# Optimization experiments

Hardware: AMD Instinct MI355X
Metric: run time of the kernel (lower is better)

## Reference

```python
import jax, jax.numpy as jnp
import numpy as np

DECAY = 0.99
EPS = 1e-05
DIM = 64
N_EMBED = 512
X_SHAPE = (32, 4096, DIM)


def setup_inputs() -> dict:
    key = jax.random.key(0)
    k1, k2 = jax.random.split(key)
    x = jax.random.normal(k1, X_SHAPE, dtype=jnp.float32)
    # codebook init uniform(-1/n_embed, 1/n_embed), as in torch .uniform_
    embed = jax.random.uniform(k2, (DIM, N_EMBED), dtype=jnp.float32,
                               minval=-1.0 / N_EMBED, maxval=1.0 / N_EMBED)
    cluster_size = jnp.zeros((N_EMBED,), dtype=jnp.float32)
    embed_avg = embed.copy()
    return {"x": x, "embed": embed, "cluster_size": cluster_size, "embed_avg": embed_avg}


def reference(x, embed, cluster_size, embed_avg):
    dim, n_embed = embed.shape
    flatten = x.reshape(-1, dim)  # [N, dim]
    # squared euclidean distance to each code: ||f||^2 - 2 f.E + ||E||^2  -> [N, n_embed]
    dist = (jnp.sum(flatten * flatten, axis=1, keepdims=True)
            - 2.0 * (flatten @ embed)
            + jnp.sum(embed * embed, axis=0, keepdims=True))
    embed_ind_flat = jnp.argmin(dist, axis=1)  # [N]
    embed_ind = embed_ind_flat.reshape(x.shape[:-1])
    quantize = jnp.take(embed.T, embed_ind_flat, axis=0).reshape(x.shape)

    # --- training-mode EMA buffer updates (no gradient flows; torch uses .data) ---
    f_sg = jax.lax.stop_gradient(flatten)
    # onehot.sum(0) == histogram of assignments; flatten.T @ onehot == segment_sum
    onehot_sum = jnp.zeros((n_embed,), dtype=x.dtype).at[embed_ind_flat].add(1.0)
    embed_sum = jax.ops.segment_sum(f_sg, embed_ind_flat, num_segments=n_embed).T  # [dim, n_embed]
    new_cluster_size = cluster_size * DECAY + (1.0 - DECAY) * onehot_sum
    new_embed_avg = embed_avg * DECAY + (1.0 - DECAY) * embed_sum
    n = jnp.sum(new_cluster_size)
    cs = (new_cluster_size + EPS) / (n + n_embed * EPS) * n
    new_embed = new_embed_avg / cs[None, :]

    diff = jnp.mean(jnp.square(jax.lax.stop_gradient(quantize) - x))
    quantize_st = x + jax.lax.stop_gradient(quantize - x)  # straight-through
    return quantize_st, diff, embed_ind, new_embed, new_cluster_size, new_embed_avg
```

## Files before the change

### kernel.cpp

```cpp
#include <hip/hip_runtime.h>

#define NVEC  131072
#define DIM   64
#define K     512
#define DECAYF 0.99f
#define OMDF   0.01f
#define EPSF   1e-5f
#define VPB   128
#define NBLK_ASSIGN (NVEC / VPB)

#define Q_OFF    0
#define DIFF_OFF 8388608
#define IND_OFF  8388609
#define NE_OFF   8519681
#define NCS_OFF  8552449
#define NEA_OFF  8552961

#define ET_OFF    0
#define C_OFF     32768
#define DPART_OFF 33280
#define INDI_OFF  35328
#define PCNT_OFF  166400
#define PESUM_OFF 168448
#define NSH_OFF   299520

__global__ __launch_bounds__(256) void vq_prep(const float* __restrict__ embed,
                                               float* __restrict__ ws) {
    #pragma clang fp contract(off)
    int j = blockIdx.x * 256 + threadIdx.x;
    float c = 0.0f;
    for (int d = 0; d < DIM; ++d) {
        float v = embed[d * K + j];
        ws[ET_OFF + j * DIM + d] = v;
        float t = v * v;
        c = c + t;
    }
    ws[C_OFF + j] = c;
}

__global__ __launch_bounds__(256)
__attribute__((amdgpu_waves_per_eu(3)))
void vq_assign(
    const float* __restrict__ x,
    const float* __restrict__ ET,
    const float* __restrict__ C,
    int*   __restrict__ indI,
    float* __restrict__ dpart,
    float* __restrict__ out)
{
    #pragma clang fp contract(off)
    __shared__ float sda[4][64], sdb[4][64];
    __shared__ int   sia[4][64], sib[4][64];
    __shared__ int   sba[64], sbb[64];
    __shared__ float wdl[4];

    int lane = threadIdx.x & 63;
    int wq   = __builtin_amdgcn_readfirstlane(threadIdx.x >> 6);
    int va   = blockIdx.x * VPB + lane;
    int vb   = va + 64;
    const float* fxa = x + (size_t)va * DIM;
    const float* fxb = x + (size_t)vb * DIM;

    float fa[DIM], fb[DIM];
    #pragma unroll
    for (int k = 0; k < DIM / 4; ++k) {
        float4 t = ((const float4*)fxa)[k];
        fa[4*k+0] = t.x; fa[4*k+1] = t.y; fa[4*k+2] = t.z; fa[4*k+3] = t.w;
    }
    #pragma unroll
    for (int k = 0; k < DIM / 4; ++k) {
        float4 t = ((const float4*)fxb)[k];
        fb[4*k+0] = t.x; fb[4*k+1] = t.y; fb[4*k+2] = t.z; fb[4*k+3] = t.w;
    }

    #define PIN16(a, b) asm volatile("" \
        : "+v"(a[(b)+0]),  "+v"(a[(b)+1]),  "+v"(a[(b)+2]),  "+v"(a[(b)+3]), \
          "+v"(a[(b)+4]),  "+v"(a[(b)+5]),  "+v"(a[(b)+6]),  "+v"(a[(b)+7]), \
          "+v"(a[(b)+8]),  "+v"(a[(b)+9]),  "+v"(a[(b)+10]), "+v"(a[(b)+11]), \
          "+v"(a[(b)+12]), "+v"(a[(b)+13]), "+v"(a[(b)+14]), "+v"(a[(b)+15]))
    PIN16(fa, 0); PIN16(fa, 16); PIN16(fa, 32); PIN16(fa, 48);
    PIN16(fb, 0); PIN16(fb, 16); PIN16(fb, 32); PIN16(fb, 48);
    #undef PIN16

    float ra[8], rb[8];
    #pragma unroll
    for (int k = 0; k < 8; ++k) { ra[k] = fa[k] * fa[k]; rb[k] = fb[k] * fb[k]; }
    #pragma unroll
    for (int b = 1; b < 8; ++b) {
        #pragma unroll
        for (int k = 0; k < 8; ++k) {
            float t0 = fa[8*b + k] * fa[8*b + k];
            ra[k] = ra[k] + t0;
            float t1 = fb[8*b + k] * fb[8*b + k];
            rb[k] = rb[k] + t1;
        }
    }
    float Aa = ((ra[0] + ra[1]) + (ra[2] + ra[3])) + ((ra[4] + ra[5]) + (ra[6] + ra[7]));
    float Ab = ((rb[0] + rb[1]) + (rb[2] + rb[3])) + ((rb[4] + rb[5]) + (rb[6] + rb[7]));

    const float* eseg = ET + (size_t)wq * 128 * DIM;
    const float* Cseg = C + wq * 128;
    float bda = 3.0e38f, bdb = 3.0e38f;
    int   bia = wq * 128, bib = wq * 128;
    #pragma unroll 1
    for (int jj = 0; jj < 128; ++jj) {
        const float* e = eseg + jj * DIM;
        float ma = 0.0f, mb = 0.0f;
        #pragma unroll
        for (int d = 0; d < DIM; ++d) {
            float ev = e[d];
            ma = __builtin_fmaf(fa[d], ev, ma);
            mb = __builtin_fmaf(fb[d], ev, mb);
        }
        int j = wq * 128 + jj;
        float Cv = Cseg[jj];
        float t1a = 2.0f * ma;
        float t2a = Aa - t1a;
        float da  = t2a + Cv;
        float t1b = 2.0f * mb;
        float t2b = Ab - t1b;
        float db  = t2b + Cv;
        if (da < bda) { bda = da; bia = j; }
        if (db < bdb) { bdb = db; bib = j; }
    }

    sda[wq][lane] = bda; sia[wq][lane] = bia;
    sdb[wq][lane] = bdb; sib[wq][lane] = bib;
    __syncthreads();

    if (wq == 0) {
        float bd = sda[0][lane]; int bi = sia[0][lane];
        #pragma unroll
        for (int q = 1; q < 4; ++q) {
            float d2 = sda[q][lane]; int i2 = sia[q][lane];
            if (d2 < bd || (d2 == bd && i2 < bi)) { bd = d2; bi = i2; }
        }
        sba[lane] = bi;
        out[IND_OFF + va] = (float)bi;
        indI[va] = bi;

        bd = sdb[0][lane]; bi = sib[0][lane];
        #pragma unroll
        for (int q = 1; q < 4; ++q) {
            float d2 = sdb[q][lane]; int i2 = sib[q][lane];
            if (d2 < bd || (d2 == bd && i2 < bi)) { bd = d2; bi = i2; }
        }
        sbb[lane] = bi;
        out[IND_OFF + vb] = (float)bi;
        indI[vb] = bi;
    }
    __syncthreads();

    float dl = 0.0f;
    if (wq == 0) {
        int bsel = sba[lane];
        const float4* qr = (const float4*)(ET + (size_t)bsel * DIM);
        float4* orow = (float4*)(out + Q_OFF + (size_t)va * DIM);
        #pragma unroll
        for (int k = 0; k < 16; ++k) {
            float4 tq = qr[k];
            float r0 = tq.x - fa[4*k+0];
            float r1 = tq.y - fa[4*k+1];
            float r2 = tq.z - fa[4*k+2];
            float r3 = tq.w - fa[4*k+3];
            dl = __builtin_fmaf(r0, r0, dl); dl = __builtin_fmaf(r1, r1, dl);
            dl = __builtin_fmaf(r2, r2, dl); dl = __builtin_fmaf(r3, r3, dl);
            orow[k] = tq;
        }
    } else if (wq == 1) {
        int bsel = sbb[lane];
        const float4* qr = (const float4*)(ET + (size_t)bsel * DIM);
        float4* orow = (float4*)(out + Q_OFF + (size_t)vb * DIM);
        #pragma unroll
        for (int k = 0; k < 16; ++k) {
            float4 tq = qr[k];
            float r0 = tq.x - fb[4*k+0];
            float r1 = tq.y - fb[4*k+1];
            float r2 = tq.z - fb[4*k+2];
            float r3 = tq.w - fb[4*k+3];
            dl = __builtin_fmaf(r0, r0, dl); dl = __builtin_fmaf(r1, r1, dl);
            dl = __builtin_fmaf(r2, r2, dl); dl = __builtin_fmaf(r3, r3, dl);
            orow[k] = tq;
        }
    }

    #pragma unroll
    for (int off = 32; off > 0; off >>= 1) dl += __shfl_down(dl, off);
    if (lane == 0) wdl[wq] = dl;
    __syncthreads();
    if (threadIdx.x == 0)
        dpart[blockIdx.x] = ((wdl[0] + wdl[1]) + (wdl[2] + wdl[3]));
}

__global__ __launch_bounds__(512) void vq_stats(
    const float* __restrict__ x,
    const int* __restrict__ indI,
    float* __restrict__ pcnt,
    float* __restrict__ pesum)
{
    __shared__ float p[8][DIM];
    __shared__ float c[8];
    int j    = blockIdx.x >> 2;
    int q    = blockIdx.x & 3;
    int lane = threadIdx.x & 63;
    int w    = __builtin_amdgcn_readfirstlane(threadIdx.x >> 6);

    int seg  = q * 8 + w;
    int base = seg * (NVEC / 32);

    float acc = 0.0f;
    int   cnt = 0;
    for (int i = 0; i < NVEC / 32; i += 256) {
        int4 idv = ((const int4*)(indI + base + i))[lane];
        unsigned long long m0 = __ballot(idv.x == j);
        unsigned long long m1 = __ballot(idv.y == j);
        unsigned long long m2 = __ballot(idv.z == j);
        unsigned long long m3 = __ballot(idv.w == j);
        cnt += (int)(__popcll(m0) + __popcll(m1) + __popcll(m2) + __popcll(m3));
        while (m0) { int b = __builtin_ctzll(m0); m0 &= m0 - 1;
                     acc += x[(size_t)(base + i + 4*b + 0) * DIM + lane]; }
        while (m1) { int b = __builtin_ctzll(m1); m1 &= m1 - 1;
                     acc += x[(size_t)(base + i + 4*b + 1) * DIM + lane]; }
        while (m2) { int b = __builtin_ctzll(m2); m2 &= m2 - 1;
                     acc += x[(size_t)(base + i + 4*b + 2) * DIM + lane]; }
        while (m3) { int b = __builtin_ctzll(m3); m3 &= m3 - 1;
                     acc += x[(size_t)(base + i + 4*b + 3) * DIM + lane]; }
    }
    p[w][lane] = acc;
    if (lane == 0) c[w] = (float)cnt;
    __syncthreads();
    if (w == 0) {
        float s = ((p[0][lane] + p[1][lane]) + (p[2][lane] + p[3][lane]))
                + ((p[4][lane] + p[5][lane]) + (p[6][lane] + p[7][lane]));
        pesum[((size_t)q * K + j) * DIM + lane] = s;
        if (lane == 0)
            pcnt[q * K + j] = ((c[0] + c[1]) + (c[2] + c[3]))
                            + ((c[4] + c[5]) + (c[6] + c[7]));
    }
}

__global__ __launch_bounds__(512) void vq_finalize1(
    const float* __restrict__ cluster_size,
    float* __restrict__ ws,
    float* __restrict__ out)
{
    __shared__ float wsum[8];
    __shared__ float dsum_sh[8];
    int j = threadIdx.x;

    float cj = ((ws[PCNT_OFF + 0*K + j] + ws[PCNT_OFF + 1*K + j])
              + (ws[PCNT_OFF + 2*K + j] + ws[PCNT_OFF + 3*K + j]));
    float ncs = DECAYF * cluster_size[j] + OMDF * cj;
    out[NCS_OFF + j] = ncs;

    float dsum = 0.0f;
    #pragma unroll
    for (int k = 0; k < NBLK_ASSIGN / 512; ++k)
        dsum += ws[DPART_OFF + k * 512 + j];

    float s = ncs;
    #pragma unroll
    for (int off = 32; off > 0; off >>= 1) {
        s    += __shfl_down(s, off);
        dsum += __shfl_down(dsum, off);
    }
    if ((j & 63) == 0) { wsum[j >> 6] = s; dsum_sh[j >> 6] = dsum; }
    __syncthreads();
    if (j == 0) {
        float n = 0.f, dtot = 0.f;
        #pragma unroll
        for (int w = 0; w < 8; ++w) { n += wsum[w]; dtot += dsum_sh[w]; }
        ws[NSH_OFF] = n;
        out[DIFF_OFF] = dtot * (1.0f / 8388608.0f);
    }
}

__global__ __launch_bounds__(512) void vq_finalize2(
    const float* __restrict__ embed_avg,
    const float* __restrict__ ws,
    float* __restrict__ out)
{
    int d = blockIdx.x;
    int j = threadIdx.x;

    float ncs = out[NCS_OFF + j];
    float n   = ws[NSH_OFF];
    float csz = (ncs + EPSF) / (n + (float)K * EPSF) * n;

    float es = ((ws[PESUM_OFF + ((size_t)0*K + j) * DIM + d]
               + ws[PESUM_OFF + ((size_t)1*K + j) * DIM + d])
              + (ws[PESUM_OFF + ((size_t)2*K + j) * DIM + d]
               + ws[PESUM_OFF + ((size_t)3*K + j) * DIM + d]));
    float ea = DECAYF * embed_avg[d * K + j] + OMDF * es;
    out[NEA_OFF + d * K + j] = ea;
    out[NE_OFF  + d * K + j] = ea / csz;
}

extern "C" void kernel_launch(void* const* d_in, const int* in_sizes, int n_in,
                              void* d_out, int out_size, void* d_ws, size_t ws_size,
                              hipStream_t stream) {
    const float* x            = (const float*)d_in[0];
    const float* embed        = (const float*)d_in[1];
    const float* cluster_size = (const float*)d_in[2];
    const float* embed_avg    = (const float*)d_in[3];
    float* out = (float*)d_out;
    float* ws  = (float*)d_ws;
    int*   indI = (int*)(ws + INDI_OFF);

    vq_prep<<<K / 256, 256, 0, stream>>>(embed, ws);
    vq_assign<<<NBLK_ASSIGN, 256, 0, stream>>>(
        x, ws + ET_OFF, ws + C_OFF, indI, ws + DPART_OFF, out);
    vq_stats<<<K * 4, 512, 0, stream>>>(
        x, indI, ws + PCNT_OFF, ws + PESUM_OFF);
    vq_finalize1<<<1, K, 0, stream>>>(cluster_size, ws, out);
    vq_finalize2<<<DIM, K, 0, stream>>>(embed_avg, ws, out);
}
```

Baseline: 262.8 us.

## Process four codes per stats block and fuse the two finalize kernels

The stats kernel now handles four codebook entries per block. Each loaded index vector is tested against all four codes, which cuts the re-reads of the index array and the block count by four. The two finalize kernels become one: every block recomputes the new cluster sizes and their total, so one launch and one global round trip go away. In exchange each block does fewer, more serial ballot loops, and the total reduction is done redundantly in all 64 finalize blocks.

New measurement: 268.8 us. +2.3%, slower.

```diff
diff --git a/kernel.cpp b/kernel.cpp
--- a/kernel.cpp
+++ b/kernel.cpp
@@ -198,65 +198,85 @@
     float* __restrict__ pcnt,
     float* __restrict__ pesum)
 {
-    __shared__ float p[8][DIM];
-    __shared__ float c[8];
-    int j    = blockIdx.x >> 2;
+    __shared__ float p[4][8][DIM];
+    __shared__ float c[4][8];
+    int jg   = blockIdx.x >> 2;
     int q    = blockIdx.x & 3;
     int lane = threadIdx.x & 63;
     int w    = __builtin_amdgcn_readfirstlane(threadIdx.x >> 6);
+    int j0   = jg * 4;
 
     int seg  = q * 8 + w;
     int base = seg * (NVEC / 32);
 
-    float acc = 0.0f;
-    int   cnt = 0;
+    float acc[4] = {0.0f, 0.0f, 0.0f, 0.0f};
+    int   cnt[4] = {0, 0, 0, 0};
     for (int i = 0; i < NVEC / 32; i += 256) {
         int4 idv = ((const int4*)(indI + base + i))[lane];
-        unsigned long long m0 = __ballot(idv.x == j);
-        unsigned long long m1 = __ballot(idv.y == j);
-        unsigned long long m2 = __ballot(idv.z == j);
-        unsigned long long m3 = __ballot(idv.w == j);
-        cnt += (int)(__popcll(m0) + __popcll(m1) + __popcll(m2) + __popcll(m3));
-        while (m0) { int b = __builtin_ctzll(m0); m0 &= m0 - 1;
-                     acc += x[(size_t)(base + i + 4*b + 0) * DIM + lane]; }
-        while (m1) { int b = __builtin_ctzll(m1); m1 &= m1 - 1;
-                     acc += x[(size_t)(base + i + 4*b + 1) * DIM + lane]; }
-        while (m2) { int b = __builtin_ctzll(m2); m2 &= m2 - 1;
-                     acc += x[(size_t)(base + i + 4*b + 2) * DIM + lane]; }
-        while (m3) { int b = __builtin_ctzll(m3); m3 &= m3 - 1;
-                     acc += x[(size_t)(base + i + 4*b + 3) * DIM + lane]; }
-    }
-    p[w][lane] = acc;
-    if (lane == 0) c[w] = (float)cnt;
+        #pragma unroll
+        for (int jj = 0; jj < 4; ++jj) {
+            int j = j0 + jj;
+            unsigned long long m0 = __ballot(idv.x == j);
+            unsigned long long m1 = __ballot(idv.y == j);
+            unsigned long long m2 = __ballot(idv.z == j);
+            unsigned long long m3 = __ballot(idv.w == j);
+            cnt[jj] += (int)(__popcll(m0) + __popcll(m1)
+                           + __popcll(m2) + __popcll(m3));
+            while (m0) { int b = __builtin_ctzll(m0); m0 &= m0 - 1;
+                         acc[jj] += x[(size_t)(base + i + 4*b + 0) * DIM + lane]; }
+            while (m1) { int b = __builtin_ctzll(m1); m1 &= m1 - 1;
+                         acc[jj] += x[(size_t)(base + i + 4*b + 1) * DIM + lane]; }
+            while (m2) { int b = __builtin_ctzll(m2); m2 &= m2 - 1;
+                         acc[jj] += x[(size_t)(base + i + 4*b + 2) * DIM + lane]; }
+            while (m3) { int b = __builtin_ctzll(m3); m3 &= m3 - 1;
+                         acc[jj] += x[(size_t)(base + i + 4*b + 3) * DIM + lane]; }
+        }
+    }
+    #pragma unroll
+    for (int jj = 0; jj < 4; ++jj) {
+        p[jj][w][lane] = acc[jj];
+        if (lane == 0) c[jj][w] = (float)cnt[jj];
+    }
     __syncthreads();
     if (w == 0) {
-        float s = ((p[0][lane] + p[1][lane]) + (p[2][lane] + p[3][lane]))
-                + ((p[4][lane] + p[5][lane]) + (p[6][lane] + p[7][lane]));
-        pesum[((size_t)q * K + j) * DIM + lane] = s;
-        if (lane == 0)
-            pcnt[q * K + j] = ((c[0] + c[1]) + (c[2] + c[3]))
-                            + ((c[4] + c[5]) + (c[6] + c[7]));
-    }
-}
-
-__global__ __launch_bounds__(512) void vq_finalize1(
+        #pragma unroll
+        for (int jj = 0; jj < 4; ++jj) {
+            float s = ((p[jj][0][lane] + p[jj][1][lane])
+                     + (p[jj][2][lane] + p[jj][3][lane]))
+                    + ((p[jj][4][lane] + p[jj][5][lane])
+                     + (p[jj][6][lane] + p[jj][7][lane]));
+            pesum[((size_t)q * K + (j0 + jj)) * DIM + lane] = s;
+            if (lane == 0)
+                pcnt[q * K + (j0 + jj)] =
+                    ((c[jj][0] + c[jj][1]) + (c[jj][2] + c[jj][3]))
+                  + ((c[jj][4] + c[jj][5]) + (c[jj][6] + c[jj][7]));
+        }
+    }
+}
+
+__global__ __launch_bounds__(512) void vq_finalize(
     const float* __restrict__ cluster_size,
-    float* __restrict__ ws,
+    const float* __restrict__ embed_avg,
+    const float* __restrict__ ws,
     float* __restrict__ out)
 {
     __shared__ float wsum[8];
     __shared__ float dsum_sh[8];
+    __shared__ float n_sh;
+    int d = blockIdx.x;
     int j = threadIdx.x;
 
     float cj = ((ws[PCNT_OFF + 0*K + j] + ws[PCNT_OFF + 1*K + j])
               + (ws[PCNT_OFF + 2*K + j] + ws[PCNT_OFF + 3*K + j]));
     float ncs = DECAYF * cluster_size[j] + OMDF * cj;
-    out[NCS_OFF + j] = ncs;
+    if (d == 0) out[NCS_OFF + j] = ncs;
 
     float dsum = 0.0f;
-    #pragma unroll
-    for (int k = 0; k < NBLK_ASSIGN / 512; ++k)
-        dsum += ws[DPART_OFF + k * 512 + j];
+    if (d == 0) {
+        #pragma unroll
+        for (int k = 0; k < NBLK_ASSIGN / 512; ++k)
+            dsum += ws[DPART_OFF + k * 512 + j];
+    }
 
     float s = ncs;
     #pragma unroll
@@ -270,21 +290,11 @@
         float n = 0.f, dtot = 0.f;
         #pragma unroll
         for (int w = 0; w < 8; ++w) { n += wsum[w]; dtot += dsum_sh[w]; }
-        ws[NSH_OFF] = n;
-        out[DIFF_OFF] = dtot * (1.0f / 8388608.0f);
-    }
-}
-
-__global__ __launch_bounds__(512) void vq_finalize2(
-    const float* __restrict__ embed_avg,
-    const float* __restrict__ ws,
-    float* __restrict__ out)
-{
-    int d = blockIdx.x;
-    int j = threadIdx.x;
-
-    float ncs = out[NCS_OFF + j];
-    float n   = ws[NSH_OFF];
+        n_sh = n;
+        if (d == 0) out[DIFF_OFF] = dtot * (1.0f / 8388608.0f);
+    }
+    __syncthreads();
+    float n   = n_sh;
     float csz = (ncs + EPSF) / (n + (float)K * EPSF) * n;
 
     float es = ((ws[PESUM_OFF + ((size_t)0*K + j) * DIM + d]
@@ -310,8 +320,7 @@
     vq_prep<<<K / 256, 256, 0, stream>>>(embed, ws);
     vq_assign<<<NBLK_ASSIGN, 256, 0, stream>>>(
         x, ws + ET_OFF, ws + C_OFF, indI, ws + DPART_OFF, out);
-    vq_stats<<<K * 4, 512, 0, stream>>>(
+    vq_stats<<<(K / 4) * 4, 512, 0, stream>>>(
         x, indI, ws + PCNT_OFF, ws + PESUM_OFF);
-    vq_finalize1<<<1, K, 0, stream>>>(cluster_size, ws, out);
-    vq_finalize2<<<DIM, K, 0, stream>>>(embed_avg, ws, out);
-}
+    vq_finalize<<<DIM, K, 0, stream>>>(cluster_size, embed_avg, ws, out);
+}
```
